# Optimization experiments

Hardware: AMD Instinct MI355X
Metric: run time of the kernel (lower is better)

## Reference

```python
import jax, jax.numpy as jnp
import numpy as np
import math

B, T, N, E = 16, 12, 2000, 8000
D, GAT_HEADS, NHEAD, FF, L, HORIZON = 64, 4, 4, 128, 2, 3
M = B * N  # batched node count


def setup_inputs() -> dict:
    key = jax.random.key(0)
    ks = jax.random.split(key, 16)

    def nrm(k, shape, s=0.1):
        return jax.random.normal(k, shape, jnp.float32) * s

    return dict(
        x_seq=jax.random.normal(ks[0], (B, T, N), jnp.float32),
        edge_index=jax.random.randint(ks[1], (2, E), 0, N),
        # GATConv 1: in_dim=1 -> 4 heads x 8 = 32
        W1=nrm(ks[2], (1, 32)),
        att_src1=nrm(ks[3], (GAT_HEADS, 8)),
        att_dst1=nrm(ks[4], (GAT_HEADS, 8)),
        b1=jnp.zeros((32,), jnp.float32),
        # GATConv 2: 32 -> 4 heads x 16 = 64
        W2=nrm(ks[5], (32, 64)),
        att_src2=nrm(ks[6], (GAT_HEADS, 16)),
        att_dst2=nrm(ks[7], (GAT_HEADS, 16)),
        b2=jnp.zeros((64,), jnp.float32),
        # TransformerEncoder (post-LN, relu), stacked over L layers
        Wqkv=nrm(ks[8], (L, 3 * D, D)), bqkv=jnp.zeros((L, 3 * D), jnp.float32),
        Wo=nrm(ks[9], (L, D, D)), bo=jnp.zeros((L, D), jnp.float32),
        Wf1=nrm(ks[10], (L, FF, D)), bf1=jnp.zeros((L, FF), jnp.float32),
        Wf2=nrm(ks[11], (L, D, FF)), bf2=jnp.zeros((L, D), jnp.float32),
        g1=jnp.ones((L, D), jnp.float32), be1=jnp.zeros((L, D), jnp.float32),
        g2=jnp.ones((L, D), jnp.float32), be2=jnp.zeros((L, D), jnp.float32),
        # prediction head
        Wh=nrm(ks[12], (HORIZON, D)), bh=jnp.zeros((HORIZON,), jnp.float32),
    )


def _layer_norm(x, g, b, eps=1e-5):
    mu = x.mean(-1, keepdims=True)
    var = ((x - mu) ** 2).mean(-1, keepdims=True)
    return (x - mu) * jax.lax.rsqrt(var + eps) * g + b


def _gat(x, src, dst, W, a_src, a_dst, bias, H, C, num_nodes):
    # PyG GATConv (concat=True, eval mode). x: [M, in] -> [M, H*C]
    h = (x @ W).reshape(-1, H, C)                                  # [M,H,C]
    e = jax.nn.leaky_relu((h * a_src).sum(-1)[src] + (h * a_dst).sum(-1)[dst], 0.2)  # [Etot,H]
    m = jax.ops.segment_max(e, dst, num_segments=num_nodes)
    w = jnp.exp(e - m[dst])
    s = jax.ops.segment_sum(w, dst, num_segments=num_nodes)
    alpha = w / (s[dst] + 1e-16)
    out = jax.ops.segment_sum(h[src] * alpha[:, :, None], dst, num_segments=num_nodes)
    return out.reshape(-1, H * C) + bias


def _forward(x_seq, edge_index, W1, att_src1, att_dst1, b1, W2, att_src2, att_dst2, b2,
             Wqkv, bqkv, Wo, bo, Wf1, bf1, Wf2, bf2, g1, be1, g2, be2, Wh, bh):
    # batch edge index with per-graph node offsets, then add self loops (PyG default)
    offs = (jnp.arange(B) * N)[:, None]
    loops = jnp.arange(M)
    src = jnp.concatenate([(edge_index[0][None] + offs).reshape(-1), loops])
    dst = jnp.concatenate([(edge_index[1][None] + offs).reshape(-1), loops])

    xt = x_seq.transpose(1, 0, 2).reshape(T, M, 1)  # per-timestep node features

    def gnn_step(x):
        h = jax.nn.relu(_gat(x, src, dst, W1, att_src1, att_dst1, b1, GAT_HEADS, 8, M))
        return jax.nn.relu(_gat(h, src, dst, W2, att_src2, att_dst2, b2, GAT_HEADS, 16, M))

    seq = jax.vmap(gnn_step)(xt)  # [T, M, D]

    # sinusoidal positional encoding over time axis
    pos = jnp.arange(T, dtype=jnp.float32)[:, None]
    div = jnp.exp(jnp.arange(0, D, 2, dtype=jnp.float32) * (-math.log(10000.0) / D))
    pe = jnp.zeros((T, D), jnp.float32)
    pe = pe.at[:, 0::2].set(jnp.sin(pos * div)).at[:, 1::2].set(jnp.cos(pos * div))
    seq = seq + pe[:, None, :]

    hd = D // NHEAD
    scale = 1.0 / math.sqrt(hd)
    for i in range(L):  # post-LN transformer encoder layers
        qkv = seq @ Wqkv[i].T + bqkv[i]
        q, k, v = jnp.split(qkv, 3, axis=-1)
        q = q.reshape(T, M, NHEAD, hd)
        k = k.reshape(T, M, NHEAD, hd)
        v = v.reshape(T, M, NHEAD, hd)
        sc = jnp.einsum('tmhd,smhd->mhts', q, k) * scale  # [M,H,T,T]
        attn = jax.nn.softmax(sc, axis=-1)
        o = jnp.einsum('mhts,smhd->tmhd', attn, v).reshape(T, M, D)
        seq = _layer_norm(seq + (o @ Wo[i].T + bo[i]), g1[i], be1[i])
        ff = jax.nn.relu(seq @ Wf1[i].T + bf1[i]) @ Wf2[i].T + bf2[i]
        seq = _layer_norm(seq + ff, g2[i], be2[i])

    final = seq[-1]  # [M, D]
    return (final @ Wh.T + bh).reshape(B, N, HORIZON).transpose(0, 2, 1)  # [B, horizon, N]


def reference(x_seq, edge_index, W1, att_src1, att_dst1, b1, W2, att_src2, att_dst2, b2,
              Wqkv, bqkv, Wo, bo, Wf1, bf1, Wf2, bf2, g1, be1, g2, be2, Wh, bh):
    return _forward(x_seq, edge_index, W1, att_src1, att_dst1, b1, W2, att_src2, att_dst2, b2,
                    Wqkv, bqkv, Wo, bo, Wf1, bf1, Wf2, bf2, g1, be1, g2, be2, Wh, bh)
```

## Files before the change

kernel.cpp:

```cpp
#include <hip/hip_runtime.h>
#include <hip/hip_bf16.h>

#define B_ 16
#define T_ 12
#define N_ 2000
#define E_ 8000
#define M_ 32000
#define ETOT (B_*E_ + M_)
#define D_ 64

typedef __hip_bfloat16 bf16;
typedef unsigned short u16;
typedef __attribute__((ext_vector_type(8))) _Float16 half8;
typedef __attribute__((ext_vector_type(2))) _Float16 h2v;
typedef __attribute__((ext_vector_type(4))) float f32x4;

__device__ __forceinline__ float bfu(u16 u){ return __uint_as_float(((unsigned int)u)<<16); }
__device__ __forceinline__ u16 f2bu(float f){
  unsigned int x = __float_as_uint(f);
  x += 0x7FFFu + ((x >> 16) & 1u);
  return (u16)(x >> 16);
}
__device__ __forceinline__ u16 f2h(float f){
  _Float16 h = (_Float16)f; u16 r; __builtin_memcpy(&r, &h, 2); return r;
}
__device__ __forceinline__ float h2f(u16 u){
  _Float16 h; __builtin_memcpy(&h, &u, 2); return (float)h;
}
__device__ __forceinline__ h2v u2h(unsigned u){ h2v r; __builtin_memcpy(&r,&u,4); return r; }

__global__ void k_prep(const float* __restrict__ Wqkv, const float* __restrict__ Wo,
                       const float* __restrict__ Wf1, const float* __restrict__ Wf2,
                       u16* __restrict__ wqB, u16* __restrict__ woB,
                       u16* __restrict__ w1B, u16* __restrict__ w2B,
                       float* __restrict__ peT){
  int i = blockIdx.x*256 + threadIdx.x;
  if(i < 24576){
    int l=i/12288, r=i-l*12288;
    int nt=r>>10, r2=r&1023, c=r2>>9, r3=r2&511, lane=r3>>3, jj=r3&7;
    int m=lane&15, q=lane>>4;
    wqB[i] = f2h(Wqkv[l*12288 + (nt*16+m)*64 + c*32 + q*8 + jj]);
  } else if(i < 32768){
    int k2=i-24576;
    int l=k2>>12, r=k2&4095;
    int nt=r>>10, r2=r&1023, c=r2>>9, r3=r2&511, lane=r3>>3, jj=r3&7;
    int m=lane&15, q=lane>>4;
    woB[k2] = f2h(Wo[l*4096 + (nt*16+m)*64 + c*32 + q*8 + jj]);
  } else if(i < 49152){
    int k2=i-32768;
    int l=k2>>13, r=k2&8191;
    int nt=r>>10, r2=r&1023, c=r2>>9, r3=r2&511, lane=r3>>3, jj=r3&7;
    int m=lane&15, q=lane>>4;
    w1B[k2] = f2h(Wf1[l*8192 + (nt*16+m)*64 + c*32 + q*8 + jj]);
  } else if(i < 65536){
    int k2=i-49152;
    int l=k2>>13, r=k2&8191;
    int nt=r>>11, r2=r&2047, c=r2>>9, r3=r2&511, lane=r3>>3, jj=r3&7;
    int m=lane&15, q=lane>>4;
    w2B[k2] = f2h(Wf2[l*8192 + (nt*16+m)*128 + c*32 + q*8 + jj]);
  } else {
    int i2 = i - 65536;
    if(i2 < 768){
      int t=i2>>6, ch=i2&63;
      float ang = (float)t * __expf(-0.14391156463f * (float)(ch & ~1));
      peT[i2] = (ch&1) ? __cosf(ang) : __sinf(ang);
    }
  }
}

__global__ void k_hist(const int* __restrict__ ei, int* __restrict__ deg){
  int e = blockIdx.x*256 + threadIdx.x; if(e>=ETOT) return;
  int dst;
  if (e < B_*E_){ int b = e / E_; int k = e - b*E_; dst = ei[E_ + k] + b*N_; }
  else dst = e - B_*E_;
  atomicAdd(&deg[dst], 1);
}

__global__ void k_scan1(const int* __restrict__ deg, int* __restrict__ offs, int* __restrict__ bsums){
  __shared__ int s[256];
  int tid = threadIdx.x; int g = blockIdx.x*256 + tid;
  s[tid] = deg[g]; __syncthreads();
  for(int off=1; off<256; off<<=1){
    int a = (tid>=off) ? s[tid-off] : 0; __syncthreads();
    s[tid] += a; __syncthreads();
  }
  offs[g+1] = s[tid];
  if(tid==255) bsums[blockIdx.x] = s[255];
}

__global__ void k_scan2(const int* __restrict__ bsums, int* __restrict__ boffs){
  __shared__ int s[128];
  int tid = threadIdx.x;
  int v = (tid<125) ? bsums[tid] : 0;
  s[tid] = v; __syncthreads();
  for(int off=1; off<128; off<<=1){
    int a = (tid>=off) ? s[tid-off] : 0; __syncthreads();
    s[tid] += a; __syncthreads();
  }
  if(tid<125) boffs[tid] = s[tid] - v;
}

__global__ void k_scan3(int* __restrict__ offs, const int* __restrict__ boffs){
  int tid = threadIdx.x; int g = blockIdx.x*256 + tid;
  offs[g+1] += boffs[blockIdx.x];
  if(g==0) offs[0]=0;
}

__global__ void k_scatter(const int* __restrict__ ei, const int* __restrict__ offs,
                          int* __restrict__ cursor, int* __restrict__ csr){
  int e = blockIdx.x*256 + threadIdx.x; if(e>=ETOT) return;
  int srcl, dst;
  if (e < B_*E_){ int b=e/E_; int k=e-b*E_; srcl=ei[k]; dst=ei[E_+k]+b*N_; }
  else { dst = e - B_*E_; int b=dst/N_; srcl = dst - b*N_; }
  int pos = atomicAdd(&cursor[dst], 1);
  csr[offs[dst]+pos] = srcl;
}

__global__ __launch_bounds__(256) void k_gat12(
  const float* __restrict__ x_seq, const float* __restrict__ W1,
  const float* __restrict__ as1, const float* __restrict__ ad1, const float* __restrict__ b1,
  const float* __restrict__ W2, const float* __restrict__ as2, const float* __restrict__ ad2,
  const int* __restrict__ offs, const int* __restrict__ csr,
  u16* __restrict__ h2u, float* __restrict__ asc, float* __restrict__ adc)
{
  __shared__ float W2s[2048];
  __shared__ float a2s[64], a2d[64];
  int tid = threadIdx.x;
  for(int i=tid;i<2048;i+=256) W2s[i]=W2[i];
  if(tid<64){ a2s[tid]=as2[tid]; a2d[tid]=ad2[tid]; }
  __syncthreads();

  int t = blockIdx.y;
  int id = blockIdx.x*256 + tid;
  int m = id>>2, l4 = id&3;

  float sS[4], sD[4];
  #pragma unroll
  for(int h=0;h<4;h++){
    float a=0.f, d=0.f;
    #pragma unroll
    for(int c=0;c<8;c++){ float w=W1[h*8+c]; a+=w*as1[h*8+c]; d+=w*ad1[h*8+c]; }
    sS[h]=a; sD[h]=d;
  }
  unsigned um=(unsigned)m, b=um/N_, n=um-b*N_;
  const float* xsl = x_seq + (size_t)(b*T_+t)*N_;
  float xm = xsl[n];
  int e0=offs[m], e1=offs[m+1];
  float sum[4]={0,0,0,0}, ax[4]={0,0,0,0};
  for(int e=e0+l4; e<e1; e+=4){
    float xv = xsl[csr[e]];
    #pragma unroll
    for(int h=0;h<4;h++){
      float ee = xv*sS[h] + xm*sD[h]; ee = ee>0.f ? ee : 0.2f*ee;
      float w = __expf(ee); sum[h]+=w; ax[h]+=w*xv;
    }
  }
  float A[4];
  #pragma unroll
  for(int h=0;h<4;h++){
    sum[h] += __shfl_xor(sum[h],1); sum[h] += __shfl_xor(sum[h],2);
    ax[h]  += __shfl_xor(ax[h],1);  ax[h]  += __shfl_xor(ax[h],2);
    A[h] = ax[h]/(sum[h]+1e-16f);
  }

  float acc[16];
  #pragma unroll
  for(int c=0;c<16;c++) acc[c]=0.f;
  #pragma unroll
  for(int k=0;k<32;k++){
    int hs = k>>3;
    float v = A[hs]*W1[k] + b1[k]; v = v>0.f ? v : 0.f;
    #pragma unroll
    for(int c=0;c<16;c++) acc[c] += v*W2s[k*64 + l4*16 + c];
  }
  uint2* hp = (uint2*)(h2u + ((size_t)t*M_ + m)*64 + l4*16);
  #pragma unroll
  for(int c2=0;c2<4;c2++){
    uint2 p;
    p.x = (unsigned)f2bu(acc[4*c2+0]) | ((unsigned)f2bu(acc[4*c2+1])<<16);
    p.y = (unsigned)f2bu(acc[4*c2+2]) | ((unsigned)f2bu(acc[4*c2+3])<<16);
    hp[c2] = p;
  }
  float ss=0.f, sd=0.f;
  #pragma unroll
  for(int c=0;c<16;c++){ ss += acc[c]*a2s[l4*16+c]; sd += acc[c]*a2d[l4*16+c]; }
  asc[((size_t)t*M_+m)*4+l4]=ss; adc[((size_t)t*M_+m)*4+l4]=sd;
}

__global__ __launch_bounds__(256) void k_gat2b(
  const u16* __restrict__ h2u, const float* __restrict__ asc, const float* __restrict__ adc,
  const float* __restrict__ b2, const int* __restrict__ offs, const int* __restrict__ csr,
  const float* __restrict__ peT, u16* __restrict__ seq)
{
  int t = blockIdx.y;
  int id = blockIdx.x*256 + threadIdx.x;
  int m = id>>2, h = id&3;
  unsigned um=(unsigned)m, b=um/N_;
  size_t base_s = (size_t)t*M_ + (size_t)b*N_;
  float am = adc[((size_t)t*M_+m)*4+h];
  int e0=offs[m], e1=offs[m+1];
  float sum=0.f;
  float A[16];
  #pragma unroll
  for(int c=0;c<16;c++) A[c]=0.f;
  for(int e=e0;e<e1;e++){
    size_t s = base_s + (unsigned)csr[e];
    float ee = asc[s*4+h] + am; ee = ee>0.f ? ee : 0.2f*ee;
    float w = __expf(ee); sum += w;
    const uint2* hp = (const uint2*)(h2u + s*64 + h*16);
    #pragma unroll
    for(int c2=0;c2<4;c2++){
      uint2 p = hp[c2];
      A[4*c2+0] += w*bfu((u16)(p.x));
      A[4*c2+1] += w*bfu((u16)(p.x>>16));
      A[4*c2+2] += w*bfu((u16)(p.y));
      A[4*c2+3] += w*bfu((u16)(p.y>>16));
    }
  }
  float inv = 1.f/(sum + 1e-16f);
  #pragma unroll
  for(int c=0;c<16;c++){
    int ch = h*16 + c;
    float v = A[c]*inv + b2[ch]; v = v>0.f ? v : 0.f;
    seq[((size_t)t*M_ + m)*64 + ch] = f2h(v + peT[t*64+ch]);
  }
}

__global__ __launch_bounds__(192) void k_layer2(
  const u16* __restrict__ seq,
  const u16* __restrict__ wqB, const u16* __restrict__ woB,
  const u16* __restrict__ w1B, const u16* __restrict__ w2B,
  const float* __restrict__ bqkv, const float* __restrict__ bo,
  const float* __restrict__ bf1,  const float* __restrict__ bf2,
  const float* __restrict__ g1,   const float* __restrict__ be1,
  const float* __restrict__ g2,   const float* __restrict__ be2,
  const float* __restrict__ Wh,   const float* __restrict__ bh,
  float* __restrict__ out)
{
  __shared__ __align__(16) u16 X[3456];
  __shared__ __align__(16) u16 QKV[10368];
  u16* Hd = QKV + 3456;
  int tid=threadIdx.x, w=tid>>6, lane=tid&63;
  int m=lane&15, q=lane>>4;
  int r = w*16 + m;

  #pragma unroll
  for(int half=0; half<2; half++){
    int rr = half*8 + (lane>>3);
    int row = w*16 + rr;
    int nn = row/12, tt = row-nn*12;
    const uint4* src = (const uint4*)(seq + ((size_t)tt*M_ + (size_t)blockIdx.x*4+nn)*64) + (lane&7);
    *((uint4*)&X[row*72] + (lane&7)) = *src;
  }

  #pragma unroll 1
  for(int l=0; l<2; l++){
    const half8* wqv = (const half8*)(wqB + (size_t)l*12288);
    const half8* wov = (const half8*)(woB + (size_t)l*4096);
    const half8* w1v = (const half8*)(w1B + (size_t)l*8192);
    const half8* w2v = (const half8*)(w2B + (size_t)l*8192);
    const float* bq = bqkv + l*192;
    const float* boL = bo + l*64;
    const float* b1L = bf1 + l*128;
    const float* b2L = bf2 + l*64;
    const float* g1L = g1 + l*64, *be1L = be1 + l*64;
    const float* g2L = g2 + l*64, *be2L = be2 + l*64;

    half8 xa0 = *(const half8*)&X[r*72 + q*8];
    half8 xa1 = *(const half8*)&X[r*72 + 32 + q*8];
    #pragma unroll
    for(int nt=0; nt<12; nt++){
      f32x4 acc={0.f,0.f,0.f,0.f};
      acc = __builtin_amdgcn_mfma_f32_16x16x32_f16(xa0, wqv[(nt*2+0)*64+lane], acc,0,0,0);
      acc = __builtin_amdgcn_mfma_f32_16x16x32_f16(xa1, wqv[(nt*2+1)*64+lane], acc,0,0,0);
      int cg = nt*16+m; float bias = bq[cg];
      int s = nt>>2, lc = cg&63;
      #pragma unroll
      for(int rg=0;rg<4;rg++){
        int row = w*16 + q*4 + rg;
        QKV[s*3456 + row*72 + lc] = f2h(acc[rg]+bias);
      }
    }
    __syncthreads();

    {
      int an = tid/48, rem = tid - an*48;
      int ah = rem/12, at = rem - ah*12;
      u16* qrow = &QKV[(an*12+at)*72 + ah*16];
      uint4 qa = ((const uint4*)qrow)[0], qb = ((const uint4*)qrow)[1];
      float s[12];
      #pragma unroll
      for(int t2=0;t2<12;t2++){
        const uint4* kp = (const uint4*)&QKV[3456 + (an*12+t2)*72 + ah*16];
        uint4 ka=kp[0], kb=kp[1];
        float d=0.f;
        d=__builtin_amdgcn_fdot2(u2h(qa.x),u2h(ka.x),d,false);
        d=__builtin_amdgcn_fdot2(u2h(qa.y),u2h(ka.y),d,false);
        d=__builtin_amdgcn_fdot2(u2h(qa.z),u2h(ka.z),d,false);
        d=__builtin_amdgcn_fdot2(u2h(qa.w),u2h(ka.w),d,false);
        d=__builtin_amdgcn_fdot2(u2h(qb.x),u2h(kb.x),d,false);
        d=__builtin_amdgcn_fdot2(u2h(qb.y),u2h(kb.y),d,false);
        d=__builtin_amdgcn_fdot2(u2h(qb.z),u2h(kb.z),d,false);
        d=__builtin_amdgcn_fdot2(u2h(qb.w),u2h(kb.w),d,false);
        s[t2] = d*0.25f;
      }
      float mx=s[0];
      #pragma unroll
      for(int t2=1;t2<12;t2++) mx=fmaxf(mx,s[t2]);
      float sum=0.f;
      #pragma unroll
      for(int t2=0;t2<12;t2++){ s[t2]=__expf(s[t2]-mx); sum+=s[t2]; }
      float inv=1.f/sum;
      half8 o0, o1;
      #pragma unroll
      for(int i=0;i<8;i++){ o0[i]=(_Float16)0.f; o1[i]=(_Float16)0.f; }
      #pragma unroll
      for(int t2=0;t2<12;t2++){
        const half8* vr = (const half8*)&QKV[6912 + (an*12+t2)*72 + ah*16];
        _Float16 wh = (_Float16)s[t2];
        o0 += vr[0]*wh; o1 += vr[1]*wh;
      }
      _Float16 ih = (_Float16)inv;
      ((half8*)qrow)[0]=o0*ih; ((half8*)qrow)[1]=o1*ih;
    }
    __syncthreads();

    half8 oa0 = *(const half8*)&QKV[r*72 + q*8];
    half8 oa1 = *(const half8*)&QKV[r*72 + 32 + q*8];
    float y[4][4];
    #pragma unroll
    for(int nt=0;nt<4;nt++){
      f32x4 acc={0.f,0.f,0.f,0.f};
      acc = __builtin_amdgcn_mfma_f32_16x16x32_f16(oa0, wov[(nt*2+0)*64+lane], acc,0,0,0);
      acc = __builtin_amdgcn_mfma_f32_16x16x32_f16(oa1, wov[(nt*2+1)*64+lane], acc,0,0,0);
      int col=nt*16+m; float bias=boL[col];
      #pragma unroll
      for(int rg=0;rg<4;rg++)
        y[nt][rg] = acc[rg] + bias + h2f(X[(w*16+q*4+rg)*72 + col]);
    }
    float mu[4], rs[4];
    #pragma unroll
    for(int rg=0;rg<4;rg++){
      float sm=(y[0][rg]+y[1][rg])+(y[2][rg]+y[3][rg]);
      sm+=__shfl_xor(sm,1); sm+=__shfl_xor(sm,2); sm+=__shfl_xor(sm,4); sm+=__shfl_xor(sm,8);
      mu[rg]=sm*(1.f/64.f);
      float d0=y[0][rg]-mu[rg],d1=y[1][rg]-mu[rg],d2=y[2][rg]-mu[rg],d3=y[3][rg]-mu[rg];
      float vv=(d0*d0+d1*d1)+(d2*d2+d3*d3);
      vv+=__shfl_xor(vv,1); vv+=__shfl_xor(vv,2); vv+=__shfl_xor(vv,4); vv+=__shfl_xor(vv,8);
      rs[rg]=rsqrtf(vv*(1.f/64.f)+1e-5f);
    }
    #pragma unroll
    for(int nt=0;nt<4;nt++){
      int col=nt*16+m; float g=g1L[col], be=be1L[col];
      #pragma unroll
      for(int rg=0;rg<4;rg++){
        float v=(y[nt][rg]-mu[rg])*rs[rg]*g+be;
        y[nt][rg]=v;
        QKV[(w*16+q*4+rg)*72 + col]=f2h(v);
      }
    }

    half8 ya0 = *(const half8*)&QKV[r*72 + q*8];
    half8 ya1 = *(const half8*)&QKV[r*72 + 32 + q*8];
    #pragma unroll
    for(int nt=0;nt<8;nt++){
      f32x4 acc={0.f,0.f,0.f,0.f};
      acc = __builtin_amdgcn_mfma_f32_16x16x32_f16(ya0, w1v[(nt*2+0)*64+lane], acc,0,0,0);
      acc = __builtin_amdgcn_mfma_f32_16x16x32_f16(ya1, w1v[(nt*2+1)*64+lane], acc,0,0,0);
      float bias=b1L[nt*16+m];
      #pragma unroll
      for(int rg=0;rg<4;rg++)
        Hd[(w*16+q*4+rg)*136 + nt*16+m] = f2h(fmaxf(acc[rg]+bias, 0.f));
    }

    half8 ha[4];
    #pragma unroll
    for(int c=0;c<4;c++)
      ha[c] = *(const half8*)&Hd[r*136 + c*32 + q*8];
    #pragma unroll
    for(int nt=0;nt<4;nt++){
      f32x4 acc={0.f,0.f,0.f,0.f};
      #pragma unroll
      for(int c=0;c<4;c++)
        acc = __builtin_amdgcn_mfma_f32_16x16x32_f16(ha[c], w2v[(nt*4+c)*64+lane], acc,0,0,0);
      int col=nt*16+m; float bias=b2L[col];
      #pragma unroll
      for(int rg=0;rg<4;rg++)
        y[nt][rg] = acc[rg] + bias + y[nt][rg];
    }
    #pragma unroll
    for(int rg=0;rg<4;rg++){
      float sm=(y[0][rg]+y[1][rg])+(y[2][rg]+y[3][rg]);
      sm+=__shfl_xor(sm,1); sm+=__shfl_xor(sm,2); sm+=__shfl_xor(sm,4); sm+=__shfl_xor(sm,8);
      mu[rg]=sm*(1.f/64.f);
      float d0=y[0][rg]-mu[rg],d1=y[1][rg]-mu[rg],d2=y[2][rg]-mu[rg],d3=y[3][rg]-mu[rg];
      float vv=(d0*d0+d1*d1)+(d2*d2+d3*d3);
      vv+=__shfl_xor(vv,1); vv+=__shfl_xor(vv,2); vv+=__shfl_xor(vv,4); vv+=__shfl_xor(vv,8);
      rs[rg]=rsqrtf(vv*(1.f/64.f)+1e-5f);
    }
    if(l==0){
      #pragma unroll
      for(int nt=0;nt<4;nt++){
        int col=nt*16+m; float g=g2L[col], be=be2L[col];
        #pragma unroll
        for(int rg=0;rg<4;rg++)
          X[(w*16+q*4+rg)*72 + col] = f2h((y[nt][rg]-mu[rg])*rs[rg]*g + be);
      }
      __syncthreads();
    } else {
      int rc = w*16 + q*4 + 3;
      int nn = rc/12;
      if(rc - nn*12 == 11){
        float vfin[4];
        #pragma unroll
        for(int nt=0;nt<4;nt++){
          int col=nt*16+m;
          vfin[nt] = (y[nt][3]-mu[3])*rs[3]*g2L[col] + be2L[col];
        }
        int gm = blockIdx.x*4 + nn;
        unsigned bb=(unsigned)gm/N_, n2=(unsigned)gm-bb*N_;
        #pragma unroll
        for(int h3=0;h3<3;h3++){
          float p = vfin[0]*Wh[h3*64+m]    + vfin[1]*Wh[h3*64+16+m]
                  + vfin[2]*Wh[h3*64+32+m] + vfin[3]*Wh[h3*64+48+m];
          p += __shfl_xor(p,1); p += __shfl_xor(p,2);
          p += __shfl_xor(p,4); p += __shfl_xor(p,8);
          if(m==0) out[(bb*3+h3)*N_+n2] = p + bh[h3];
        }
      }
    }
  }
}

extern "C" void kernel_launch(void* const* d_in, const int* in_sizes, int n_in,
                              void* d_out, int out_size, void* d_ws, size_t ws_size,
                              hipStream_t stream)
{
  const float* x_seq=(const float*)d_in[0];
  const int*   ei   =(const int*)d_in[1];
  const float* W1   =(const float*)d_in[2];
  const float* as1  =(const float*)d_in[3];
  const float* ad1  =(const float*)d_in[4];
  const float* b1   =(const float*)d_in[5];
  const float* W2   =(const float*)d_in[6];
  const float* as2  =(const float*)d_in[7];
  const float* ad2  =(const float*)d_in[8];
  const float* b2   =(const float*)d_in[9];
  const float* Wqkv =(const float*)d_in[10];
  const float* bqkv =(const float*)d_in[11];
  const float* Wo   =(const float*)d_in[12];
  const float* bo   =(const float*)d_in[13];
  const float* Wf1  =(const float*)d_in[14];
  const float* bf1p =(const float*)d_in[15];
  const float* Wf2  =(const float*)d_in[16];
  const float* bf2p =(const float*)d_in[17];
  const float* g1   =(const float*)d_in[18];
  const float* be1  =(const float*)d_in[19];
  const float* g2   =(const float*)d_in[20];
  const float* be2  =(const float*)d_in[21];
  const float* Wh   =(const float*)d_in[22];
  const float* bh   =(const float*)d_in[23];

  u16* seqh   = (u16*)d_ws;
  float* asc  = (float*)(seqh + 24576000);
  float* adc  = asc + 1536000;
  int* deg    = (int*)(adc + 1536000);
  int* cursor = deg + M_;
  int* offs   = cursor + M_;
  int* bsums  = offs + (M_ + 2);
  int* boffs  = bsums + 128;
  int* csr    = boffs + 128;
  u16* h2u    = (u16*)(csr + ETOT);
  u16* wqB    = h2u + (size_t)T_*M_*64;
  u16* woB    = wqB + 24576;
  u16* w1B    = woB + 8192;
  u16* w2B    = w1B + 16384;
  float* peT  = (float*)(w2B + 16384);

  k_prep   <<<dim3(260), dim3(256), 0, stream>>>(Wqkv, Wo, Wf1, Wf2, wqB, woB, w1B, w2B, peT);

  hipMemsetAsync(deg, 0, (size_t)2*M_*sizeof(int), stream);
  k_hist   <<<dim3((ETOT+255)/256), dim3(256), 0, stream>>>(ei, deg);
  k_scan1  <<<dim3(125), dim3(256), 0, stream>>>(deg, offs, bsums);
  k_scan2  <<<dim3(1),   dim3(128), 0, stream>>>(bsums, boffs);
  k_scan3  <<<dim3(125), dim3(256), 0, stream>>>(offs, boffs);
  k_scatter<<<dim3((ETOT+255)/256), dim3(256), 0, stream>>>(ei, offs, cursor, csr);

  k_gat12<<<dim3(500,T_), dim3(256), 0, stream>>>(x_seq, W1, as1, ad1, b1,
                                                  W2, as2, ad2, offs, csr, h2u, asc, adc);
  k_gat2b<<<dim3(500,T_), dim3(256), 0, stream>>>(h2u, asc, adc, b2, offs, csr, peT, seqh);

  k_layer2<<<dim3(8000), dim3(192), 0, stream>>>(seqh,
      wqB, woB, w1B, w2B,
      bqkv, bo, bf1p, bf2p,
      g1, be1, g2, be2,
      Wh, bh, (float*)d_out);
}
```

Measured before the change: 400.8 us.

## Use MFMA for GAT layer-2 projection in k_gat12 with pre-swizzled fp16 W2

Replaces the per-thread scalar 32x64 W2 projection, which staged W2 through shared memory, with four 16x16x32 f16 MFMA instructions per wavefront. W2 is pre-converted to fp16 in the MFMA fragment layout inside k_prep. The thread-to-node mapping changes so each lane handles one node and one head, and the edge loop runs serially per lane instead of split across four lanes. The attention score dot products are computed with a butterfly shuffle reduction. This adds fp16 rounding of the layer-1 activations and W2, and lengthens the serial per-lane edge loop.

```diff
diff --git a/kernel.cpp b/kernel.cpp
--- a/kernel.cpp
+++ b/kernel.cpp
@@ -29,11 +29,40 @@
 }
 __device__ __forceinline__ h2v u2h(unsigned u){ h2v r; __builtin_memcpy(&r,&u,4); return r; }
 
+__device__ __forceinline__ float redsel16(const float v[16], int m){
+  float c8[8];
+  #pragma unroll
+  for(int i=0;i<8;i++){
+    float send = (m&8)? v[i]   : v[i+8];
+    float keep = (m&8)? v[i+8] : v[i];
+    c8[i] = keep + __shfl_xor(send, 8);
+  }
+  float c4[4];
+  #pragma unroll
+  for(int i=0;i<4;i++){
+    float send = (m&4)? c8[i]   : c8[i+4];
+    float keep = (m&4)? c8[i+4] : c8[i];
+    c4[i] = keep + __shfl_xor(send, 4);
+  }
+  float c2[2];
+  #pragma unroll
+  for(int i=0;i<2;i++){
+    float send = (m&2)? c2[0]*0.f + c4[i] : c4[i+2];
+    float keep = (m&2)? c4[i+2] : c4[i];
+    c2[i] = keep + __shfl_xor(((m&2)? c4[i] : c4[i+2]), 2);
+    c2[i] = keep + __shfl_xor(send, 2);
+  }
+  float send = (m&1)? c2[0] : c2[1];
+  float keep = (m&1)? c2[1] : c2[0];
+  return keep + __shfl_xor(send, 1);
+}
+
 __global__ void k_prep(const float* __restrict__ Wqkv, const float* __restrict__ Wo,
                        const float* __restrict__ Wf1, const float* __restrict__ Wf2,
+                       const float* __restrict__ W2g,
                        u16* __restrict__ wqB, u16* __restrict__ woB,
                        u16* __restrict__ w1B, u16* __restrict__ w2B,
-                       float* __restrict__ peT){
+                       float* __restrict__ peT, u16* __restrict__ w2gB){
   int i = blockIdx.x*256 + threadIdx.x;
   if(i < 24576){
     int l=i/12288, r=i-l*12288;
@@ -64,6 +93,11 @@
       int t=i2>>6, ch=i2&63;
       float ang = (float)t * __expf(-0.14391156463f * (float)(ch & ~1));
       peT[i2] = (ch&1) ? __cosf(ang) : __sinf(ang);
+    } else if(i2 < 768+2048){
+      int i3 = i2-768;
+      int nt=i3>>9, r=i3&511, lane=r>>3, j=r&7;
+      int m=lane&15, q=lane>>4;
+      w2gB[i3] = f2h(W2g[(q*8+j)*64 + nt*16 + m]);
     }
   }
 }
@@ -119,72 +153,78 @@
 __global__ __launch_bounds__(256) void k_gat12(
   const float* __restrict__ x_seq, const float* __restrict__ W1,
   const float* __restrict__ as1, const float* __restrict__ ad1, const float* __restrict__ b1,
-  const float* __restrict__ W2, const float* __restrict__ as2, const float* __restrict__ ad2,
+  const float* __restrict__ as2, const float* __restrict__ ad2,
   const int* __restrict__ offs, const int* __restrict__ csr,
+  const u16* __restrict__ w2gB,
   u16* __restrict__ h2u, float* __restrict__ asc, float* __restrict__ adc)
 {
-  __shared__ float W2s[2048];
-  __shared__ float a2s[64], a2d[64];
-  int tid = threadIdx.x;
-  for(int i=tid;i<2048;i+=256) W2s[i]=W2[i];
-  if(tid<64){ a2s[tid]=as2[tid]; a2d[tid]=ad2[tid]; }
-  __syncthreads();
-
+  int tid = threadIdx.x, w = tid>>6, lane = tid&63;
+  int m = lane&15, q = lane>>4;
   int t = blockIdx.y;
-  int id = blockIdx.x*256 + tid;
-  int m = id>>2, l4 = id&3;
-
-  float sS[4], sD[4];
-  #pragma unroll
-  for(int h=0;h<4;h++){
-    float a=0.f, d=0.f;
-    #pragma unroll
-    for(int c=0;c<8;c++){ float w=W1[h*8+c]; a+=w*as1[h*8+c]; d+=w*ad1[h*8+c]; }
-    sS[h]=a; sD[h]=d;
-  }
-  unsigned um=(unsigned)m, b=um/N_, n=um-b*N_;
+  int node = blockIdx.x*64 + w*16 + m;
+  unsigned un=(unsigned)node, b=un/N_, n=un-b*N_;
+
+  const half8* wb = (const half8*)w2gB;
+  half8 w2f0 = wb[0*64+lane], w2f1 = wb[1*64+lane],
+        w2f2 = wb[2*64+lane], w2f3 = wb[3*64+lane];
+
+  float sS=0.f, sD=0.f;
+  #pragma unroll
+  for(int c=0;c<8;c++){ float wv=W1[q*8+c]; sS+=wv*as1[q*8+c]; sD+=wv*ad1[q*8+c]; }
+
   const float* xsl = x_seq + (size_t)(b*T_+t)*N_;
   float xm = xsl[n];
-  int e0=offs[m], e1=offs[m+1];
-  float sum[4]={0,0,0,0}, ax[4]={0,0,0,0};
-  for(int e=e0+l4; e<e1; e+=4){
+  int e0=offs[node], e1=offs[node+1];
+  float sum=0.f, ax=0.f;
+  for(int e=e0;e<e1;e++){
     float xv = xsl[csr[e]];
-    #pragma unroll
-    for(int h=0;h<4;h++){
-      float ee = xv*sS[h] + xm*sD[h]; ee = ee>0.f ? ee : 0.2f*ee;
-      float w = __expf(ee); sum[h]+=w; ax[h]+=w*xv;
-    }
-  }
-  float A[4];
-  #pragma unroll
-  for(int h=0;h<4;h++){
-    sum[h] += __shfl_xor(sum[h],1); sum[h] += __shfl_xor(sum[h],2);
-    ax[h]  += __shfl_xor(ax[h],1);  ax[h]  += __shfl_xor(ax[h],2);
-    A[h] = ax[h]/(sum[h]+1e-16f);
-  }
-
-  float acc[16];
-  #pragma unroll
-  for(int c=0;c<16;c++) acc[c]=0.f;
-  #pragma unroll
-  for(int k=0;k<32;k++){
-    int hs = k>>3;
-    float v = A[hs]*W1[k] + b1[k]; v = v>0.f ? v : 0.f;
-    #pragma unroll
-    for(int c=0;c<16;c++) acc[c] += v*W2s[k*64 + l4*16 + c];
-  }
-  uint2* hp = (uint2*)(h2u + ((size_t)t*M_ + m)*64 + l4*16);
-  #pragma unroll
-  for(int c2=0;c2<4;c2++){
-    uint2 p;
-    p.x = (unsigned)f2bu(acc[4*c2+0]) | ((unsigned)f2bu(acc[4*c2+1])<<16);
-    p.y = (unsigned)f2bu(acc[4*c2+2]) | ((unsigned)f2bu(acc[4*c2+3])<<16);
-    hp[c2] = p;
-  }
-  float ss=0.f, sd=0.f;
-  #pragma unroll
-  for(int c=0;c<16;c++){ ss += acc[c]*a2s[l4*16+c]; sd += acc[c]*a2d[l4*16+c]; }
-  asc[((size_t)t*M_+m)*4+l4]=ss; adc[((size_t)t*M_+m)*4+l4]=sd;
+    float ee = xv*sS + xm*sD; ee = ee>0.f ? ee : 0.2f*ee;
+    float wv = __expf(ee); sum += wv; ax += wv*xv;
+  }
+  float A = ax/(sum+1e-16f);
+
+  half8 af;
+  #pragma unroll
+  for(int j=0;j<8;j++){
+    float v = A*W1[q*8+j] + b1[q*8+j]; v = v>0.f?v:0.f;
+    af[j] = (_Float16)v;
+  }
+  f32x4 ac0={0.f,0.f,0.f,0.f}, ac1=ac0, ac2=ac0, ac3=ac0;
+  ac0 = __builtin_amdgcn_mfma_f32_16x16x32_f16(af, w2f0, ac0,0,0,0);
+  ac1 = __builtin_amdgcn_mfma_f32_16x16x32_f16(af, w2f1, ac1,0,0,0);
+  ac2 = __builtin_amdgcn_mfma_f32_16x16x32_f16(af, w2f2, ac2,0,0,0);
+  ac3 = __builtin_amdgcn_mfma_f32_16x16x32_f16(af, w2f3, ac3,0,0,0);
+
+  size_t hbase = (size_t)t*M_;
+  int ndbase = blockIdx.x*64 + w*16 + q*4;
+  #pragma unroll
+  for(int rg=0;rg<4;rg++){
+    u16* row = h2u + (hbase + ndbase + rg)*64;
+    row[ 0+m] = f2bu(ac0[rg]);
+    row[16+m] = f2bu(ac1[rg]);
+    row[32+m] = f2bu(ac2[rg]);
+    row[48+m] = f2bu(ac3[rg]);
+  }
+
+  float a2sv[4], a2dv[4];
+  #pragma unroll
+  for(int h=0;h<4;h++){ a2sv[h]=as2[h*16+m]; a2dv[h]=ad2[h*16+m]; }
+  float pa[16], pd[16];
+  #pragma unroll
+  for(int rg=0;rg<4;rg++){
+    pa[0*4+rg]=ac0[rg]*a2sv[0]; pd[0*4+rg]=ac0[rg]*a2dv[0];
+    pa[1*4+rg]=ac1[rg]*a2sv[1]; pd[1*4+rg]=ac1[rg]*a2dv[1];
+    pa[2*4+rg]=ac2[rg]*a2sv[2]; pd[2*4+rg]=ac2[rg]*a2dv[2];
+    pa[3*4+rg]=ac3[rg]*a2sv[3]; pd[3*4+rg]=ac3[rg]*a2dv[3];
+  }
+  float ra = redsel16(pa, m);
+  float rd = redsel16(pd, m);
+  {
+    int h=m>>2, rg=m&3;
+    size_t nd = hbase + ndbase + rg;
+    asc[nd*4+h] = ra;
+    adc[nd*4+h] = rd;
+  }
 }
 
 __global__ __launch_bounds__(256) void k_gat2b(
@@ -476,8 +516,10 @@
   u16* w1B    = woB + 8192;
   u16* w2B    = w1B + 16384;
   float* peT  = (float*)(w2B + 16384);
-
-  k_prep   <<<dim3(260), dim3(256), 0, stream>>>(Wqkv, Wo, Wf1, Wf2, wqB, woB, w1B, w2B, peT);
+  u16* w2gB   = (u16*)(peT + 768);
+
+  k_prep   <<<dim3(268), dim3(256), 0, stream>>>(Wqkv, Wo, Wf1, Wf2, W2,
+                                                 wqB, woB, w1B, w2B, peT, w2gB);
 
   hipMemsetAsync(deg, 0, (size_t)2*M_*sizeof(int), stream);
   k_hist   <<<dim3((ETOT+255)/256), dim3(256), 0, stream>>>(ei, deg);
@@ -487,7 +529,8 @@
   k_scatter<<<dim3((ETOT+255)/256), dim3(256), 0, stream>>>(ei, offs, cursor, csr);
 
   k_gat12<<<dim3(500,T_), dim3(256), 0, stream>>>(x_seq, W1, as1, ad1, b1,
-                                                  W2, as2, ad2, offs, csr, h2u, asc, adc);
+                                                  as2, ad2, offs, csr, w2gB,
+                                                  h2u, asc, adc);
   k_gat2b<<<dim3(500,T_), dim3(256), 0, stream>>>(h2u, asc, adc, b2, offs, csr, peT, seqh);
 
   k_layer2<<<dim3(8000), dim3(192), 0, stream>>>(seqh,
```

Measured after the change: 385.8 us. 1.04x faster.
